# Performance work log

Hardware: AMD Instinct MI355X
Metric: run time of the kernel (lower is better)

The kernel has to match this reference:

```python
import jax, jax.numpy as jnp
import numpy as np

B, T, M, C, H = 4, 2048, 256, 512, 8
D = C // H  # head dim = 64


def _split_heads(t, n):  # [B,N,C] -> [B,H,N,D]
    b, s, c = t.shape
    return t.reshape(b, s, H, c // H).transpose(0, 2, 1, 3)


def setup_inputs() -> dict:
    key = jax.random.key(0)
    ks = jax.random.split(key, 16)
    s = 0.02
    inp = {
        "x": jax.random.normal(ks[0], (B, T, C), jnp.float32),
        "y": jax.random.normal(ks[1], (B, M, C), jnp.float32),
        "attn_x_mask": jnp.tril(jnp.ones((T, T), jnp.int32))[None, None],  # causal [1,1,T,T]
        "Wqkv_x": jax.random.normal(ks[2], (C, 3 * C), jnp.float32) * s,
        "bqkv_x": jnp.zeros((3 * C,), jnp.float32),
        "Wqkv_y": jax.random.normal(ks[3], (C, 3 * C), jnp.float32) * s,
        "bqkv_y": jnp.zeros((3 * C,), jnp.float32),
        "Wgs": jax.random.normal(ks[4], (C, C), jnp.float32) * s,
        "bgs": jnp.zeros((C,), jnp.float32),
        "Wgc": jax.random.normal(ks[5], (C, C), jnp.float32) * s,
        "bgc": jnp.zeros((C,), jnp.float32),
        "Wp": jax.random.normal(ks[6], (C, C), jnp.float32) * s,
        "bp": jnp.zeros((C,), jnp.float32),
    }
    return inp


def reference(x, y, attn_x_mask, Wqkv_x, bqkv_x, Wqkv_y, bqkv_y, Wgs, bgs, Wgc, bgc, Wp, bp):
    b, t, c = x.shape
    _, m, _ = y.shape
    scale = 1.0 / np.sqrt(D).astype(np.float32)

    qx, kx, vx = jnp.split(x @ Wqkv_x + bqkv_x, 3, axis=-1)
    qy, ky, vy = jnp.split(y @ Wqkv_y + bqkv_y, 3, axis=-1)
    qx, kx, vx = _split_heads(qx, H), _split_heads(kx, H), _split_heads(vx, H)
    qy, ky, vy = _split_heads(qy, H), _split_heads(ky, H), _split_heads(vy, H)

    # self-attn logits over x: [B,H,T,T]
    satt = jnp.einsum('bhtd,bhsd->bhts', qx, kx) * scale
    # cross scores y->x: [B,H,M,T]; bias = mean over M of softmax(dim=M)*scores -> [B,H,1,T]
    catt_y = jnp.einsum('bhmd,bhtd->bhmt', qy, kx) * scale
    bias = jnp.mean(jax.nn.softmax(catt_y, axis=-2) * catt_y, axis=-2, keepdims=True)
    satt = satt + bias  # broadcast over query rows
    satt = jnp.where(attn_x_mask == 0, -jnp.inf, satt)
    satt = jax.nn.softmax(satt, axis=-1)

    # cross-attn x->y: [B,H,T,M]
    catt = jax.nn.softmax(jnp.einsum('bhtd,bhmd->bhtm', qx, ky) * scale, axis=-1)

    sval = jnp.einsum('bhts,bhsd->bhtd', satt, vx).transpose(0, 2, 1, 3).reshape(b, t, c)
    cval = jnp.einsum('bhtm,bhmd->bhtd', catt, vy).transpose(0, 2, 1, 3).reshape(b, t, c)

    sgate = jax.nn.sigmoid(sval @ Wgs + bgs)
    cgate = jax.nn.sigmoid(cval @ Wgc + bgc)
    out = (sgate * cval + cgate * sval) @ Wp + bp
    return out
```

## Files before the change

### kernel.cpp

```cpp
#include <hip/hip_runtime.h>
#include <hip/hip_bf16.h>
#include <math.h>

#define B_ 4
#define T_ 2048
#define M_ 256
#define C_ 512
#define H_ 8
#define D_ 64
#define TC3 1536
#define QSCALE 0.125f

typedef _Float16 half_t;
typedef _Float16 half8 __attribute__((ext_vector_type(8)));
typedef _Float16 half4 __attribute__((ext_vector_type(4)));
typedef float floatx4 __attribute__((ext_vector_type(4)));

__device__ __forceinline__ void gload_lds16(const half_t* g, half_t* lds) {
  __builtin_amdgcn_global_load_lds(
      (const __attribute__((address_space(1))) unsigned int*)g,
      (__attribute__((address_space(3))) unsigned int*)(unsigned)(unsigned long long)(void*)lds,
      16, 0, 0);
}

__device__ __forceinline__ floatx4 mfma16(half8 a, half8 b, floatx4 c) {
  return __builtin_amdgcn_mfma_f32_16x16x32_f16(a, b, c, 0, 0, 0);
}
__device__ __forceinline__ floatx4 mfma16k16(half4 a, half4 b, floatx4 c) {
  return __builtin_amdgcn_mfma_f32_16x16x16f16(a, b, c, 0, 0, 0);
}

__device__ __forceinline__ half8 frag64(const half_t* lds, int row, int kc, int quad) {
  int slot = ((kc << 2) + quad) ^ (row & 7);
  return *(const half8*)(lds + row * 64 + slot * 8);
}
__device__ __forceinline__ half8 frag32(const half_t* lds, int row, int quad) {
  int slot = quad ^ ((row >> 1) & 3);
  return *(const half8*)(lds + row * 32 + slot * 8);
}

__global__ __launch_bounds__(256) void conv_all(
    const float* x, half_t* xo, const float* y, half_t* yo,
    const float* w0, const float* w1, const float* w2, const float* w3, const float* w4,
    half_t* o0, half_t* o1, half_t* o2, half_t* o3, half_t* o4) {
  __shared__ float tile[32][33];
  const int tid = threadIdx.x;
  if (blockIdx.x < 2304) {
    int blk = blockIdx.x;
    const float* src; half_t* dst; int N;
    if (blk < 768)       { src = w0; dst = o0; N = 1536; }
    else if (blk < 1536) { src = w1; dst = o1; N = 1536; blk -= 768; }
    else if (blk < 1792) { src = w2; dst = o2; N = 512;  blk -= 1536; }
    else if (blk < 2048) { src = w3; dst = o3; N = 512;  blk -= 1792; }
    else                 { src = w4; dst = o4; N = 512;  blk -= 2048; }
    const int ntx = N >> 5;
    const int tk = blk / ntx, tn = blk % ntx;
    const int r = tid >> 3, c = (tid & 7) * 4;
    float4 v = *(const float4*)(src + (size_t)(tk * 32 + r) * N + tn * 32 + c);
    tile[r][c] = v.x; tile[r][c + 1] = v.y; tile[r][c + 2] = v.z; tile[r][c + 3] = v.w;
    __syncthreads();
    half4 h;
#pragma unroll
    for (int j = 0; j < 4; ++j) h[j] = (half_t)tile[c + j][r];
    *(half4*)(dst + (size_t)(tn * 32 + r) * 512 + tk * 32 + c) = h;
  } else {
    const int nx = B_ * T_ * C_, ny = B_ * M_ * C_;
    const int n4x = nx >> 2, tot = n4x + (ny >> 2);
    int i = (blockIdx.x - 2304) * 256 + tid;
    const int stride = (gridDim.x - 2304) * 256;
    for (; i < tot; i += stride) {
      const float4* s; half_t* d; int idx;
      if (i < n4x) { s = (const float4*)x; d = xo; idx = i; }
      else { s = (const float4*)y; d = yo; idx = i - n4x; }
      float4 v = s[idx];
      half4 h; h[0] = (half_t)v.x; h[1] = (half_t)v.y; h[2] = (half_t)v.z; h[3] = (half_t)v.w;
      *(half4*)(d + idx * 4) = h;
    }
  }
}

struct GemmAcc { floatx4 a[4][4]; };

__device__ __forceinline__ void gemm_core(
    const half_t* __restrict__ A, const half_t* __restrict__ Wt,
    int rowBase, int colBase, GemmAcc& g,
    half_t* As, half_t* Bs, int tid) {
  const int lane = tid & 63, wave = tid >> 6;
  const int wm = wave >> 1, wn = wave & 1;
  const int qd = lane >> 4, lr = lane & 15;
  const int sr = lane >> 2, sc = lane & 3;
#pragma unroll
  for (int mi = 0; mi < 4; ++mi)
#pragma unroll
    for (int ni = 0; ni < 4; ++ni)
#pragma unroll
      for (int r = 0; r < 4; ++r) g.a[mi][ni][r] = 0.f;
  for (int k0 = 0; k0 < 512; k0 += 32) {
    __syncthreads();
#pragma unroll
    for (int i = 0; i < 2; ++i) {
      int r = wave * 32 + i * 16 + sr;
      int cs = sc ^ ((r >> 1) & 3);
      gload_lds16(A + (size_t)(rowBase + r) * 512 + k0 + cs * 8, As + (wave * 32 + i * 16) * 32);
      gload_lds16(Wt + (size_t)(colBase + r) * 512 + k0 + cs * 8, Bs + (wave * 32 + i * 16) * 32);
    }
    __syncthreads();
    half8 af[4], bf[4];
#pragma unroll
    for (int mi = 0; mi < 4; ++mi) af[mi] = frag32(As, wm * 64 + mi * 16 + lr, qd);
#pragma unroll
    for (int ni = 0; ni < 4; ++ni) bf[ni] = frag32(Bs, wn * 64 + ni * 16 + lr, qd);
#pragma unroll
    for (int mi = 0; mi < 4; ++mi)
#pragma unroll
      for (int ni = 0; ni < 4; ++ni)
        g.a[mi][ni] = mfma16(af[mi], bf[ni], g.a[mi][ni]);
  }
}

__global__ __launch_bounds__(256) void gemm_qkvt(
    const half_t* __restrict__ x16, const half_t* __restrict__ y16,
    const half_t* __restrict__ WxT, const half_t* __restrict__ WyT,
    const float* __restrict__ bqx, const float* __restrict__ bqy,
    half_t* __restrict__ qkvx, half_t* __restrict__ qkvy,
    half_t* __restrict__ vTx, half_t* __restrict__ vTy) {
  __shared__ __align__(16) half_t As[128 * 32];
  __shared__ __align__(16) half_t Bs[128 * 32];
  const int tid = threadIdx.x, lane = tid & 63, wave = tid >> 6;
  const int wm = wave >> 1, wn = wave & 1;
  const int qd = lane >> 4, lr = lane & 15;
  const int bxi = blockIdx.x;
  const half_t* A; const half_t* Wt; const float* bias; half_t* out;
  int rowBase, colBase, N; bool vt;
  if (bxi < 576) {
    vt = false; N = 1024;
    colBase = (bxi & 7) * 128;
    int ry = bxi >> 3;
    if (ry < 64) { A = x16; Wt = WxT; bias = bqx; out = qkvx; rowBase = ry * 128; }
    else { A = y16; Wt = WyT; bias = bqy; out = qkvy; rowBase = (ry - 64) * 128; }
  } else {
    vt = true;
    int i = bxi - 576;
    int xx = i % 18; int rest = i / 18;
    int yy = rest & 3, zz = rest >> 2;
    rowBase = yy * 128;
    if (xx < 16) {
      A = WxT + (size_t)1024 * 512; Wt = x16 + (size_t)zz * T_ * C_; bias = bqx + 1024;
      out = vTx + (size_t)zz * C_ * T_; N = T_; colBase = xx * 128;
    } else {
      A = WyT + (size_t)1024 * 512; Wt = y16 + (size_t)zz * M_ * C_; bias = bqy + 1024;
      out = vTy + (size_t)zz * C_ * M_; N = M_; colBase = (xx - 16) * 128;
    }
  }
  GemmAcc g;
  gemm_core(A, Wt, rowBase, colBase, g, As, Bs, tid);
  if (!vt) {
#pragma unroll
    for (int ni = 0; ni < 4; ++ni) {
      int col = colBase + wn * 64 + ni * 16 + lr;
      float csc = (col < 512) ? QSCALE : 1.f;
      float bc = bias[col];
#pragma unroll
      for (int mi = 0; mi < 4; ++mi) {
        int row0 = rowBase + wm * 64 + mi * 16 + qd * 4;
#pragma unroll
        for (int r = 0; r < 4; ++r)
          out[(size_t)(row0 + r) * 1024 + col] = (half_t)((g.a[mi][ni][r] + bc) * csc);
      }
    }
  } else {
#pragma unroll
    for (int ni = 0; ni < 4; ++ni) {
      int col = colBase + wn * 64 + ni * 16 + lr;
#pragma unroll
      for (int mi = 0; mi < 4; ++mi) {
        int row0 = rowBase + wm * 64 + mi * 16 + qd * 4;
#pragma unroll
        for (int r = 0; r < 4; ++r)
          out[(size_t)(row0 + r) * N + col] = (half_t)(g.a[mi][ni][r] + bias[row0 + r]);
      }
    }
  }
}

template <bool USE_BIAS, bool DO_A, bool DIAG_A, bool DIAG_B>
__device__ __forceinline__ void attn_tile_dual(
    const half_t* __restrict__ Ks, const half_t* __restrict__ Vts,
    const float* __restrict__ Bsh, const half8* qfA, const half8* qfB,
    floatx4* oA, floatx4& lacA, floatx4* oB, floatx4& lacB,
    int qd, int lr, int thresh) {
  floatx4 sA[4], sB[4];
#pragma unroll
  for (int ks = 0; ks < 4; ++ks)
#pragma unroll
    for (int r = 0; r < 4; ++r) { sA[ks][r] = 0.f; sB[ks][r] = 0.f; }
#pragma unroll
  for (int kc = 0; kc < 2; ++kc) {
#pragma unroll
    for (int ks = 0; ks < 4; ++ks) {
      half8 kfr = frag64(Ks, ks * 16 + lr, kc, qd);
      if (DO_A) sA[ks] = mfma16(kfr, qfA[kc], sA[ks]);
      sB[ks] = mfma16(kfr, qfB[kc], sB[ks]);
    }
  }
  half4 pA[4], pB[4];
#pragma unroll
  for (int ks = 0; ks < 4; ++ks) {
    floatx4 bf;
    if (USE_BIAS) bf = *(const floatx4*)(Bsh + ks * 16 + qd * 4);
#pragma unroll
    for (int r = 0; r < 4; ++r) {
      int keyl = ks * 16 + qd * 4 + r;
      if (DO_A) {
        float t = USE_BIAS ? (sA[ks][r] + bf[r]) : sA[ks][r];
        float p1 = __expf(t);
        if (DIAG_A && keyl > thresh) p1 = 0.f;
        pA[ks][r] = (half_t)p1;
      }
      float t2 = USE_BIAS ? (sB[ks][r] + bf[r]) : sB[ks][r];
      float p2 = __expf(t2);
      if (DIAG_B && keyl > thresh) p2 = 0.f;
      pB[ks][r] = (half_t)p2;
    }
  }
  const half4 ones4 = {(half_t)1.f, (half_t)1.f, (half_t)1.f, (half_t)1.f};
#pragma unroll
  for (int ks = 0; ks < 4; ++ks) {
    int slot = (ks * 2 + (qd >> 1)) ^ (lr & 7);
    const half_t* vbase = Vts + slot * 8 + (qd & 1) * 4;
#pragma unroll
    for (int dt = 0; dt < 4; ++dt) {
      half4 vf = *(const half4*)(vbase + (dt * 16 + lr) * 64);
      if (DO_A) oA[dt] = mfma16k16(pA[ks], vf, oA[dt]);
      oB[dt] = mfma16k16(pB[ks], vf, oB[dt]);
    }
    if (DO_A) lacA = mfma16k16(pA[ks], ones4, lacA);
    lacB = mfma16k16(pB[ks], ones4, lacB);
  }
}

__device__ __forceinline__ void attn_store2(
    half_t* __restrict__ dst, const floatx4* o, floatx4 lac,
    int b, int qbase, int h, int qd, int lr) {
  floatx4 inv;
#pragma unroll
  for (int r = 0; r < 4; ++r) inv[r] = 1.f / lac[r];
#pragma unroll
  for (int dt = 0; dt < 4; ++dt)
#pragma unroll
    for (int r = 0; r < 4; ++r)
      dst[(size_t)(b * T_ + qbase + qd * 4 + r) * C_ + h * D_ + dt * 16 + lr] =
          (half_t)(o[dt][r] * inv[r]);
}

__global__ __launch_bounds__(256) void bias_cross(
    const half_t* __restrict__ qkvx, const half_t* __restrict__ qkvy,
    const half_t* __restrict__ vTy, float* __restrict__ biasb,
    half_t* __restrict__ cval) {
  __shared__ __align__(16) half_t smem[24576];
  const int tid = threadIdx.x, lane = tid & 63, wave = tid >> 6;
  const int qd = lane >> 4, lr = lane & 15;
  const int rr = lane >> 3, cc = lane & 7;
  if (blockIdx.x < 512) {
    half_t* Qy = smem;
    half_t* Kx = smem + 16384;
    const int bh = blockIdx.x >> 4;
    const int tb = (blockIdx.x & 15) * 128;
    const int b = bh >> 3, h = bh & 7;
#pragma unroll
    for (int j = 0; j < 8; ++j) {
      int r = wave * 64 + j * 8 + rr;
      int cs = cc ^ (r & 7);
      gload_lds16(qkvy + (size_t)(b * M_ + r) * 1024 + h * D_ + cs * 8,
                  Qy + (wave * 64 + j * 8) * 64);
    }
#pragma unroll
    for (int j = 0; j < 4; ++j) {
      int r = wave * 32 + j * 8 + rr;
      int cs = cc ^ (r & 7);
      gload_lds16(qkvx + (size_t)(b * T_ + tb + r) * 1024 + C_ + h * D_ + cs * 8,
                  Kx + (wave * 32 + j * 8) * 64);
    }
    __syncthreads();
    half8 kf[2][2];
#pragma unroll
    for (int nt = 0; nt < 2; ++nt)
#pragma unroll
      for (int kc = 0; kc < 2; ++kc)
        kf[nt][kc] = frag64(Kx, wave * 32 + nt * 16 + lr, kc, qd);
    float ls[2] = {0.f, 0.f}, wsp[2] = {0.f, 0.f};
    for (int mt = 0; mt < 16; ++mt) {
      half8 af[2];
#pragma unroll
      for (int kc = 0; kc < 2; ++kc) af[kc] = frag64(Qy, mt * 16 + lr, kc, qd);
#pragma unroll
      for (int nt = 0; nt < 2; ++nt) {
        floatx4 s;
#pragma unroll
        for (int r = 0; r < 4; ++r) s[r] = 0.f;
#pragma unroll
        for (int kc = 0; kc < 2; ++kc) s = mfma16(af[kc], kf[nt][kc], s);
#pragma unroll
        for (int r = 0; r < 4; ++r) {
          float e = __expf(s[r]);
          ls[nt] += e;
          wsp[nt] += e * s[r];
        }
      }
    }
#pragma unroll
    for (int nt = 0; nt < 2; ++nt) {
      ls[nt] += __shfl_xor(ls[nt], 16, 64);
      ls[nt] += __shfl_xor(ls[nt], 32, 64);
      wsp[nt] += __shfl_xor(wsp[nt], 16, 64);
      wsp[nt] += __shfl_xor(wsp[nt], 32, 64);
    }
    if (qd == 0) {
#pragma unroll
      for (int nt = 0; nt < 2; ++nt)
        biasb[bh * T_ + tb + wave * 32 + nt * 16 + lr] = wsp[nt] / (256.f * ls[nt]);
    }
  } else {
    half_t* Qs  = smem;
    half_t* Ks  = smem + 8192;
    half_t* Vts = smem + 12288;
    const int idx = blockIdx.x - 512;
    const int bh = idx >> 4;
    const int qb = (idx & 15) * 128;
    const int b = bh >> 3, h = bh & 7;
#pragma unroll
    for (int j = 0; j < 4; ++j) {
      int row = wave * 32 + j * 8 + rr;
      int cs = cc ^ (row & 7);
      gload_lds16(qkvx + (size_t)(b * T_ + qb + row) * 1024 + h * D_ + cs * 8,
                  Qs + (wave * 32 + j * 8) * 64);
    }
    __syncthreads();
    half8 qfA[2], qfB[2];
#pragma unroll
    for (int kc = 0; kc < 2; ++kc) {
      qfA[kc] = frag64(Qs, wave * 32 + lr, kc, qd);
      qfB[kc] = frag64(Qs, wave * 32 + 16 + lr, kc, qd);
    }
    floatx4 oA[4], oB[4], lacA, lacB;
#pragma unroll
    for (int dt = 0; dt < 4; ++dt)
#pragma unroll
      for (int r = 0; r < 4; ++r) { oA[dt][r] = 0.f; oB[dt][r] = 0.f; }
#pragma unroll
    for (int r = 0; r < 4; ++r) { lacA[r] = 0.f; lacB[r] = 0.f; }
    for (int kt = 0; kt < 4; ++kt) {
      const int kb = kt * 64;
      __syncthreads();
#pragma unroll
      for (int j = 0; j < 2; ++j) {
        int row = wave * 16 + j * 8 + rr;
        int cs = cc ^ (row & 7);
        gload_lds16(qkvy + (size_t)(b * M_ + kb + row) * 1024 + C_ + h * D_ + cs * 8,
                    Ks + (wave * 16 + j * 8) * 64);
        gload_lds16(vTy + ((size_t)bh * 64 + row) * M_ + kb + cs * 8,
                    Vts + (wave * 16 + j * 8) * 64);
      }
      __syncthreads();
      attn_tile_dual<false, true, false, false>(Ks, Vts, nullptr, qfA, qfB,
                                                oA, lacA, oB, lacB, qd, lr, 0);
    }
    attn_store2(cval, oA, lacA, b, qb + wave * 32, h, qd, lr);
    attn_store2(cval, oB, lacB, b, qb + wave * 32 + 16, h, qd, lr);
  }
}

__global__ __launch_bounds__(256) void self_attn_part(
    const half_t* __restrict__ qkv, const half_t* __restrict__ vT,
    const float* __restrict__ biasb, float* __restrict__ partO,
    float* __restrict__ partL) {
  __shared__ __align__(16) half_t Qs[128 * 64];
  __shared__ __align__(16) half_t Ks[64 * 64];
  __shared__ __align__(16) half_t Vts[64 * 64];
  __shared__ __align__(16) float Bsh[64];
  const int tid = threadIdx.x, lane = tid & 63, wave = tid >> 6;
  const int half_ = blockIdx.x & 1;
  const int p = (blockIdx.x >> 1) & 15;
  const int bh = blockIdx.x >> 5;
  const int b = bh >> 3, h = bh & 7;
  const int qbL = p * 64, qbH = (31 - p) * 64;
  const int qd = lane >> 4, lr = lane & 15;
  const int rr = lane >> 3, cc = lane & 7;

#pragma unroll
  for (int j = 0; j < 4; ++j) {
    int rowIdx = wave * 32 + j * 8 + rr;
    int grow = (rowIdx < 64) ? (qbL + rowIdx) : (qbH + rowIdx - 64);
    int cs = cc ^ (rowIdx & 7);
    gload_lds16(qkv + (size_t)(b * T_ + grow) * 1024 + h * D_ + cs * 8,
                Qs + (wave * 32 + j * 8) * 64);
  }
  __syncthreads();
  half8 qfA[2], qfB[2];
#pragma unroll
  for (int kc = 0; kc < 2; ++kc) {
    qfA[kc] = frag64(Qs, wave * 16 + lr, kc, qd);
    qfB[kc] = frag64(Qs, 64 + wave * 16 + lr, kc, qd);
  }

  floatx4 oA[4], oB[4], lacA, lacB;
#pragma unroll
  for (int dt = 0; dt < 4; ++dt)
#pragma unroll
    for (int r = 0; r < 4; ++r) { oA[dt][r] = 0.f; oB[dt][r] = 0.f; }
#pragma unroll
  for (int r = 0; r < 4; ++r) { lacA[r] = 0.f; lacB[r] = 0.f; }
  const int thresh = wave * 16 + lr;
  const int ktEnd = 31 - p;

  for (int kt = half_; kt <= ktEnd; kt += 2) {
    const int kb = kt * 64;
    __syncthreads();
#pragma unroll
    for (int j = 0; j < 2; ++j) {
      int row = wave * 16 + j * 8 + rr;
      int cs = cc ^ (row & 7);
      gload_lds16(qkv + (size_t)(b * T_ + kb + row) * 1024 + C_ + h * D_ + cs * 8,
                  Ks + (wave * 16 + j * 8) * 64);
      gload_lds16(vT + ((size_t)bh * 64 + row) * T_ + kb + cs * 8,
                  Vts + (wave * 16 + j * 8) * 64);
    }
    if (tid < 64) Bsh[tid] = biasb[bh * T_ + kb + tid];
    __syncthreads();

    if (kt < p)
      attn_tile_dual<true, true, false, false>(Ks, Vts, Bsh, qfA, qfB, oA, lacA, oB, lacB, qd, lr, thresh);
    else if (kt == p)
      attn_tile_dual<true, true, true, false>(Ks, Vts, Bsh, qfA, qfB, oA, lacA, oB, lacB, qd, lr, thresh);
    else if (kt < ktEnd)
      attn_tile_dual<true, false, false, false>(Ks, Vts, Bsh, qfA, qfB, oA, lacA, oB, lacB, qd, lr, thresh);
    else
      attn_tile_dual<true, false, false, true>(Ks, Vts, Bsh, qfA, qfB, oA, lacA, oB, lacB, qd, lr, thresh);
  }

  const long rbase = ((long)(half_ * 32 + bh) * 16 + p) * 128;
#pragma unroll
  for (int g = 0; g < 2; ++g) {
    const floatx4* o = g ? oB : oA;
    floatx4 lac = g ? lacB : lacA;
    long rowb = rbase + g * 64 + wave * 16;
#pragma unroll
    for (int dt = 0; dt < 4; ++dt)
#pragma unroll
      for (int r = 0; r < 4; ++r)
        partO[(rowb + qd * 4 + r) * 64 + dt * 16 + lr] = o[dt][r];
    if (lr == 0) {
#pragma unroll
      for (int r = 0; r < 4; ++r) partL[rowb + qd * 4 + r] = lac[r];
    }
  }
}

__global__ __launch_bounds__(256) void self_reduce(
    const float* __restrict__ partO, const float* __restrict__ partL,
    half_t* __restrict__ sval) {
  const int bh = blockIdx.x >> 4;
  const int p = blockIdx.x & 15;
  const int b = bh >> 3, h = bh & 7;
  const int tid = threadIdx.x;
  const int c4 = tid & 15;
  const long hstrO = 32L * 16 * 128 * 64;
  const long hstrL = 32L * 16 * 128;
  const float* base0 = partO + ((long)bh * 16 + p) * 128 * 64;
  const float* base1 = base0 + hstrO;
  const float* l0 = partL + ((long)bh * 16 + p) * 128;
  const float* l1 = l0 + hstrL;
#pragma unroll
  for (int pass = 0; pass < 8; ++pass) {
    int qrow = pass * 16 + (tid >> 4);
    float4 v0 = *(const float4*)(base0 + (long)qrow * 64 + c4 * 4);
    float4 v1 = *(const float4*)(base1 + (long)qrow * 64 + c4 * 4);
    float inv = 1.f / (l0[qrow] + l1[qrow]);
    int t = (qrow < 64) ? (p * 64 + qrow) : ((31 - p) * 64 + (qrow - 64));
    half4 o;
    o[0] = (half_t)((v0.x + v1.x) * inv);
    o[1] = (half_t)((v0.y + v1.y) * inv);
    o[2] = (half_t)((v0.z + v1.z) * inv);
    o[3] = (half_t)((v0.w + v1.w) * inv);
    *(half4*)(sval + (size_t)(b * T_ + t) * 512 + h * 64 + c4 * 4) = o;
  }
}

__global__ __launch_bounds__(256) void gate_gemm64(
    const half_t* __restrict__ sv, const half_t* __restrict__ cv,
    const half_t* __restrict__ W1, const half_t* __restrict__ W2,
    const float* __restrict__ b1, const float* __restrict__ b2,
    half_t* __restrict__ z) {
  __shared__ __align__(16) half_t S1[64 * 32];
  __shared__ __align__(16) half_t S2[64 * 32];
  __shared__ __align__(16) half_t B1s[128 * 32];
  __shared__ __align__(16) half_t B2s[128 * 32];
  const int tid = threadIdx.x, lane = tid & 63, wave = tid >> 6;
  const int wm = wave >> 1, wn = wave & 1;
  const int rowBase = blockIdx.y * 64, colBase = blockIdx.x * 128;
  const int qd = lane >> 4, lr = lane & 15;
  const int sr = lane >> 2, sc = lane & 3;

  floatx4 a1[2][4], a2[2][4];
#pragma unroll
  for (int mi = 0; mi < 2; ++mi)
#pragma unroll
    for (int ni = 0; ni < 4; ++ni)
#pragma unroll
      for (int r = 0; r < 4; ++r) { a1[mi][ni][r] = 0.f; a2[mi][ni][r] = 0.f; }

  for (int k0 = 0; k0 < 512; k0 += 32) {
    __syncthreads();
    {
      int rA = wave * 16 + sr;
      int csA = sc ^ ((rA >> 1) & 3);
      gload_lds16(sv + (size_t)(rowBase + rA) * 512 + k0 + csA * 8, S1 + (wave * 16) * 32);
      gload_lds16(cv + (size_t)(rowBase + rA) * 512 + k0 + csA * 8, S2 + (wave * 16) * 32);
#pragma unroll
      for (int i = 0; i < 2; ++i) {
        int rB = i * 64 + wave * 16 + sr;
        int csB = sc ^ ((rB >> 1) & 3);
        gload_lds16(W1 + (size_t)(colBase + rB) * 512 + k0 + csB * 8, B1s + (i * 64 + wave * 16) * 32);
        gload_lds16(W2 + (size_t)(colBase + rB) * 512 + k0 + csB * 8, B2s + (i * 64 + wave * 16) * 32);
      }
    }
    __syncthreads();
    half8 af1[2], af2[2], bf1[4], bf2[4];
#pragma unroll
    for (int mi = 0; mi < 2; ++mi) {
      af1[mi] = frag32(S1, wm * 32 + mi * 16 + lr, qd);
      af2[mi] = frag32(S2, wm * 32 + mi * 16 + lr, qd);
    }
#pragma unroll
    for (int ni = 0; ni < 4; ++ni) {
      bf1[ni] = frag32(B1s, wn * 64 + ni * 16 + lr, qd);
      bf2[ni] = frag32(B2s, wn * 64 + ni * 16 + lr, qd);
    }
#pragma unroll
    for (int mi = 0; mi < 2; ++mi)
#pragma unroll
      for (int ni = 0; ni < 4; ++ni) {
        a1[mi][ni] = mfma16(af1[mi], bf1[ni], a1[mi][ni]);
        a2[mi][ni] = mfma16(af2[mi], bf2[ni], a2[mi][ni]);
      }
  }

#pragma unroll
  for (int ni = 0; ni < 4; ++ni) {
    int col = colBase + wn * 64 + ni * 16 + lr;
    float g1b = b1[col], g2b = b2[col];
#pragma unroll
    for (int mi = 0; mi < 2; ++mi) {
      int row0 = rowBase + wm * 32 + mi * 16 + qd * 4;
#pragma unroll
      for (int r = 0; r < 4; ++r) {
        size_t idx = (size_t)(row0 + r) * 512 + col;
        float sg1 = 1.f / (1.f + __expf(-(a1[mi][ni][r] + g1b)));
        float sg2 = 1.f / (1.f + __expf(-(a2[mi][ni][r] + g2b)));
        z[idx] = (half_t)(sg1 * (float)cv[idx] + sg2 * (float)sv[idx]);
      }
    }
  }
}

__global__ __launch_bounds__(256) void gemm_final64(
    const half_t* __restrict__ A, const half_t* __restrict__ Wt,
    const float* __restrict__ bias, float* __restrict__ Cout) {
  __shared__ __align__(16) half_t As[64 * 32];
  __shared__ __align__(16) half_t Bs[128 * 32];
  const int tid = threadIdx.x, lane = tid & 63, wave = tid >> 6;
  const int wm = wave >> 1, wn = wave & 1;
  const int rowBase = blockIdx.y * 64, colBase = blockIdx.x * 128;
  const int qd = lane >> 4, lr = lane & 15;
  const int sr = lane >> 2, sc = lane & 3;

  floatx4 acc[2][4];
#pragma unroll
  for (int mi = 0; mi < 2; ++mi)
#pragma unroll
    for (int ni = 0; ni < 4; ++ni)
#pragma unroll
      for (int r = 0; r < 4; ++r) acc[mi][ni][r] = 0.f;

  for (int k0 = 0; k0 < 512; k0 += 32) {
    __syncthreads();
    {
      int rA = wave * 16 + sr;
      int csA = sc ^ ((rA >> 1) & 3);
      gload_lds16(A + (size_t)(rowBase + rA) * 512 + k0 + csA * 8, As + (wave * 16) * 32);
#pragma unroll
      for (int i = 0; i < 2; ++i) {
        int rB = i * 64 + wave * 16 + sr;
        int csB = sc ^ ((rB >> 1) & 3);
        gload_lds16(Wt + (size_t)(colBase + rB) * 512 + k0 + csB * 8, Bs + (i * 64 + wave * 16) * 32);
      }
    }
    __syncthreads();
    half8 af[2], bf[4];
#pragma unroll
    for (int mi = 0; mi < 2; ++mi) af[mi] = frag32(As, wm * 32 + mi * 16 + lr, qd);
#pragma unroll
    for (int ni = 0; ni < 4; ++ni) bf[ni] = frag32(Bs, wn * 64 + ni * 16 + lr, qd);
#pragma unroll
    for (int mi = 0; mi < 2; ++mi)
#pragma unroll
      for (int ni = 0; ni < 4; ++ni)
        acc[mi][ni] = mfma16(af[mi], bf[ni], acc[mi][ni]);
  }

#pragma unroll
  for (int ni = 0; ni < 4; ++ni) {
    int col = colBase + wn * 64 + ni * 16 + lr;
    float bc = bias[col];
#pragma unroll
    for (int mi = 0; mi < 2; ++mi) {
      int row0 = rowBase + wm * 32 + mi * 16 + qd * 4;
#pragma unroll
      for (int r = 0; r < 4; ++r)
        Cout[(size_t)(row0 + r) * 512 + col] = acc[mi][ni][r] + bc;
    }
  }
}

extern "C" void kernel_launch(void* const* d_in, const int* in_sizes, int n_in,
                              void* d_out, int out_size, void* d_ws, size_t ws_size,
                              hipStream_t stream) {
  (void)in_sizes; (void)n_in; (void)out_size; (void)ws_size;
  const float* x      = (const float*)d_in[0];
  const float* y      = (const float*)d_in[1];
  const float* Wqkv_x = (const float*)d_in[3];
  const float* bqkv_x = (const float*)d_in[4];
  const float* Wqkv_y = (const float*)d_in[5];
  const float* bqkv_y = (const float*)d_in[6];
  const float* Wgs    = (const float*)d_in[7];
  const float* bgs    = (const float*)d_in[8];
  const float* Wgc    = (const float*)d_in[9];
  const float* bgc    = (const float*)d_in[10];
  const float* Wp     = (const float*)d_in[11];
  const float* bp     = (const float*)d_in[12];
  float* out = (float*)d_out;

  half_t* h = (half_t*)d_ws;
  half_t* x16    = h;  h += (size_t)B_ * T_ * C_;
  half_t* y16    = h;  h += (size_t)B_ * M_ * C_;
  half_t* WqkvxT = h;  h += (size_t)TC3 * C_;
  half_t* WqkvyT = h;  h += (size_t)TC3 * C_;
  half_t* WgsT   = h;  h += (size_t)C_ * C_;
  half_t* WgcT   = h;  h += (size_t)C_ * C_;
  half_t* WpT    = h;  h += (size_t)C_ * C_;
  half_t* qkvx   = h;  h += (size_t)B_ * T_ * 1024;
  half_t* qkvy   = h;  h += (size_t)B_ * M_ * 1024;
  half_t* vTx    = h;  h += (size_t)B_ * C_ * T_;
  half_t* vTy    = h;  h += (size_t)B_ * C_ * M_;
  half_t* sval   = h;  h += (size_t)B_ * T_ * C_;
  half_t* cval   = h;  h += (size_t)B_ * T_ * C_;
  half_t* z      = h;  h += (size_t)B_ * T_ * C_;
  float* biasb   = (float*)h;
  float* partO   = biasb + (size_t)B_ * H_ * T_;
  float* partL   = partO + 2L * 32 * 16 * 128 * 64;

  conv_all<<<3456, 256, 0, stream>>>(x, x16, y, y16,
                                     Wqkv_x, Wqkv_y, Wgs, Wgc, Wp,
                                     WqkvxT, WqkvyT, WgsT, WgcT, WpT);

  gemm_qkvt<<<864, 256, 0, stream>>>(x16, y16, WqkvxT, WqkvyT,
                                     bqkv_x, bqkv_y, qkvx, qkvy, vTx, vTy);

  bias_cross<<<1024, 256, 0, stream>>>(qkvx, qkvy, vTy, biasb, cval);

  self_attn_part<<<1024, 256, 0, stream>>>(qkvx, vTx, biasb, partO, partL);
  self_reduce<<<512, 256, 0, stream>>>(partO, partL, sval);

  gate_gemm64<<<dim3(4, 128), 256, 0, stream>>>(sval, cval, WgsT, WgcT, bgs, bgc, z);

  gemm_final64<<<dim3(4, 128), 256, 0, stream>>>(z, WpT, bp, out);
}
```

Before: 241.1 us.

## Widen GEMM K-tiles to 64 and merge split-K self-attention into one kernel

All GEMM kernels now stage 64-wide K slices into LDS with the 8-way XOR swizzle, which halves the number of barrier-separated iterations. The self-attention partial kernel and its reduction pass are replaced by a single kernel that processes two key tiles per barrier and writes normalized output directly. This removes the fp32 partial buffers and one launch, but halves the self-attention grid to 512 blocks and raises LDS use per block. The cross-attention branch also loads two K/V tiles per synchronization.

```diff
diff --git a/kernel.cpp b/kernel.cpp
--- a/kernel.cpp
+++ b/kernel.cpp
@@ -33,10 +33,6 @@
 __device__ __forceinline__ half8 frag64(const half_t* lds, int row, int kc, int quad) {
   int slot = ((kc << 2) + quad) ^ (row & 7);
   return *(const half8*)(lds + row * 64 + slot * 8);
-}
-__device__ __forceinline__ half8 frag32(const half_t* lds, int row, int quad) {
-  int slot = quad ^ ((row >> 1) & 3);
-  return *(const half8*)(lds + row * 32 + slot * 8);
 }
 
 __global__ __launch_bounds__(256) void conv_all(
@@ -81,40 +77,43 @@
 
 struct GemmAcc { floatx4 a[4][4]; };
 
-__device__ __forceinline__ void gemm_core(
+__device__ __forceinline__ void gemm_core64(
     const half_t* __restrict__ A, const half_t* __restrict__ Wt,
     int rowBase, int colBase, GemmAcc& g,
     half_t* As, half_t* Bs, int tid) {
   const int lane = tid & 63, wave = tid >> 6;
   const int wm = wave >> 1, wn = wave & 1;
   const int qd = lane >> 4, lr = lane & 15;
-  const int sr = lane >> 2, sc = lane & 3;
+  const int rr = lane >> 3, cc = lane & 7;
+  const int cs = cc ^ rr;
 #pragma unroll
   for (int mi = 0; mi < 4; ++mi)
 #pragma unroll
     for (int ni = 0; ni < 4; ++ni)
 #pragma unroll
       for (int r = 0; r < 4; ++r) g.a[mi][ni][r] = 0.f;
-  for (int k0 = 0; k0 < 512; k0 += 32) {
-    __syncthreads();
-#pragma unroll
-    for (int i = 0; i < 2; ++i) {
-      int r = wave * 32 + i * 16 + sr;
-      int cs = sc ^ ((r >> 1) & 3);
-      gload_lds16(A + (size_t)(rowBase + r) * 512 + k0 + cs * 8, As + (wave * 32 + i * 16) * 32);
-      gload_lds16(Wt + (size_t)(colBase + r) * 512 + k0 + cs * 8, Bs + (wave * 32 + i * 16) * 32);
-    }
-    __syncthreads();
-    half8 af[4], bf[4];
-#pragma unroll
-    for (int mi = 0; mi < 4; ++mi) af[mi] = frag32(As, wm * 64 + mi * 16 + lr, qd);
-#pragma unroll
-    for (int ni = 0; ni < 4; ++ni) bf[ni] = frag32(Bs, wn * 64 + ni * 16 + lr, qd);
-#pragma unroll
-    for (int mi = 0; mi < 4; ++mi)
-#pragma unroll
-      for (int ni = 0; ni < 4; ++ni)
-        g.a[mi][ni] = mfma16(af[mi], bf[ni], g.a[mi][ni]);
+  for (int k0 = 0; k0 < 512; k0 += 64) {
+    __syncthreads();
+#pragma unroll
+    for (int j = 0; j < 4; ++j) {
+      int row = wave * 32 + j * 8 + rr;
+      gload_lds16(A + (size_t)(rowBase + row) * 512 + k0 + cs * 8, As + (wave * 32 + j * 8) * 64);
+      gload_lds16(Wt + (size_t)(colBase + row) * 512 + k0 + cs * 8, Bs + (wave * 32 + j * 8) * 64);
+    }
+    __syncthreads();
+#pragma unroll
+    for (int kc = 0; kc < 2; ++kc) {
+      half8 af[4], bf[4];
+#pragma unroll
+      for (int mi = 0; mi < 4; ++mi) af[mi] = frag64(As, wm * 64 + mi * 16 + lr, kc, qd);
+#pragma unroll
+      for (int ni = 0; ni < 4; ++ni) bf[ni] = frag64(Bs, wn * 64 + ni * 16 + lr, kc, qd);
+#pragma unroll
+      for (int mi = 0; mi < 4; ++mi)
+#pragma unroll
+        for (int ni = 0; ni < 4; ++ni)
+          g.a[mi][ni] = mfma16(af[mi], bf[ni], g.a[mi][ni]);
+    }
   }
 }
 
@@ -124,8 +123,8 @@
     const float* __restrict__ bqx, const float* __restrict__ bqy,
     half_t* __restrict__ qkvx, half_t* __restrict__ qkvy,
     half_t* __restrict__ vTx, half_t* __restrict__ vTy) {
-  __shared__ __align__(16) half_t As[128 * 32];
-  __shared__ __align__(16) half_t Bs[128 * 32];
+  __shared__ __align__(16) half_t As[128 * 64];
+  __shared__ __align__(16) half_t Bs[128 * 64];
   const int tid = threadIdx.x, lane = tid & 63, wave = tid >> 6;
   const int wm = wave >> 1, wn = wave & 1;
   const int qd = lane >> 4, lr = lane & 15;
@@ -153,7 +152,7 @@
     }
   }
   GemmAcc g;
-  gemm_core(A, Wt, rowBase, colBase, g, As, Bs, tid);
+  gemm_core64(A, Wt, rowBase, colBase, g, As, Bs, tid);
   if (!vt) {
 #pragma unroll
     for (int ni = 0; ni < 4; ++ni) {
@@ -239,6 +238,22 @@
   }
 }
 
+__device__ __forceinline__ void attn_step(
+    int kt, int p, int ktEnd,
+    const half_t* Ks, const half_t* Vts, const float* Bsh,
+    const half8* qfA, const half8* qfB,
+    floatx4* oA, floatx4& lacA, floatx4* oB, floatx4& lacB,
+    int qd, int lr, int thresh) {
+  if (kt < p)
+    attn_tile_dual<true, true, false, false>(Ks, Vts, Bsh, qfA, qfB, oA, lacA, oB, lacB, qd, lr, thresh);
+  else if (kt == p)
+    attn_tile_dual<true, true, true, false>(Ks, Vts, Bsh, qfA, qfB, oA, lacA, oB, lacB, qd, lr, thresh);
+  else if (kt < ktEnd)
+    attn_tile_dual<true, false, false, false>(Ks, Vts, Bsh, qfA, qfB, oA, lacA, oB, lacB, qd, lr, thresh);
+  else
+    attn_tile_dual<true, false, false, true>(Ks, Vts, Bsh, qfA, qfB, oA, lacA, oB, lacB, qd, lr, thresh);
+}
+
 __device__ __forceinline__ void attn_store2(
     half_t* __restrict__ dst, const floatx4* o, floatx4 lac,
     int b, int qbase, int h, int qd, int lr) {
@@ -251,6 +266,80 @@
     for (int r = 0; r < 4; ++r)
       dst[(size_t)(b * T_ + qbase + qd * 4 + r) * C_ + h * D_ + dt * 16 + lr] =
           (half_t)(o[dt][r] * inv[r]);
+}
+
+__global__ __launch_bounds__(256) void self_attn_reg(
+    const half_t* __restrict__ qkv, const half_t* __restrict__ vT,
+    const float* __restrict__ biasb, half_t* __restrict__ sval) {
+  __shared__ __align__(16) half_t Qs[128 * 64];
+  __shared__ __align__(16) half_t Ks[2][64 * 64];
+  __shared__ __align__(16) half_t Vts[2][64 * 64];
+  __shared__ __align__(16) float Bsh[128];
+  const int tid = threadIdx.x, lane = tid & 63, wave = tid >> 6;
+  const int p = blockIdx.x & 15;
+  const int bh = blockIdx.x >> 4;
+  const int b = bh >> 3, h = bh & 7;
+  const int qbL = p * 64, qbH = (31 - p) * 64;
+  const int qd = lane >> 4, lr = lane & 15;
+  const int rr = lane >> 3, cc = lane & 7;
+  const int cs = cc ^ rr;
+
+#pragma unroll
+  for (int j = 0; j < 4; ++j) {
+    int rowIdx = wave * 32 + j * 8 + rr;
+    int grow = (rowIdx < 64) ? (qbL + rowIdx) : (qbH + rowIdx - 64);
+    gload_lds16(qkv + (size_t)(b * T_ + grow) * 1024 + h * D_ + cs * 8,
+                Qs + (wave * 32 + j * 8) * 64);
+  }
+  __syncthreads();
+  half8 qfA[2], qfB[2];
+#pragma unroll
+  for (int kc = 0; kc < 2; ++kc) {
+    qfA[kc] = frag64(Qs, wave * 16 + lr, kc, qd);
+    qfB[kc] = frag64(Qs, 64 + wave * 16 + lr, kc, qd);
+  }
+
+  floatx4 oA[4], oB[4], lacA, lacB;
+#pragma unroll
+  for (int dt = 0; dt < 4; ++dt)
+#pragma unroll
+    for (int r = 0; r < 4; ++r) { oA[dt][r] = 0.f; oB[dt][r] = 0.f; }
+#pragma unroll
+  for (int r = 0; r < 4; ++r) { lacA[r] = 0.f; lacB[r] = 0.f; }
+  const int thresh = wave * 16 + lr;
+  const int ktEnd = 31 - p;
+
+  for (int kt2 = 0; kt2 <= ktEnd; kt2 += 2) {
+    const bool two = (kt2 + 1 <= ktEnd);
+    __syncthreads();
+#pragma unroll
+    for (int j = 0; j < 2; ++j) {
+      int row = wave * 16 + j * 8 + rr;
+      gload_lds16(qkv + (size_t)(b * T_ + kt2 * 64 + row) * 1024 + C_ + h * D_ + cs * 8,
+                  Ks[0] + (wave * 16 + j * 8) * 64);
+      gload_lds16(vT + ((size_t)bh * 64 + row) * T_ + kt2 * 64 + cs * 8,
+                  Vts[0] + (wave * 16 + j * 8) * 64);
+    }
+    if (two) {
+#pragma unroll
+      for (int j = 0; j < 2; ++j) {
+        int row = wave * 16 + j * 8 + rr;
+        gload_lds16(qkv + (size_t)(b * T_ + kt2 * 64 + 64 + row) * 1024 + C_ + h * D_ + cs * 8,
+                    Ks[1] + (wave * 16 + j * 8) * 64);
+        gload_lds16(vT + ((size_t)bh * 64 + row) * T_ + kt2 * 64 + 64 + cs * 8,
+                    Vts[1] + (wave * 16 + j * 8) * 64);
+      }
+    }
+    if (tid < 128) Bsh[tid] = biasb[bh * T_ + kt2 * 64 + tid];
+    __syncthreads();
+
+    attn_step(kt2, p, ktEnd, Ks[0], Vts[0], Bsh, qfA, qfB, oA, lacA, oB, lacB, qd, lr, thresh);
+    if (two)
+      attn_step(kt2 + 1, p, ktEnd, Ks[1], Vts[1], Bsh + 64, qfA, qfB, oA, lacA, oB, lacB, qd, lr, thresh);
+  }
+
+  attn_store2(sval, oA, lacA, b, qbL + wave * 16, h, qd, lr);
+  attn_store2(sval, oB, lacB, b, qbH + wave * 16, h, qd, lr);
 }
 
 __global__ __launch_bounds__(256) void bias_cross(
@@ -261,6 +350,7 @@
   const int tid = threadIdx.x, lane = tid & 63, wave = tid >> 6;
   const int qd = lane >> 4, lr = lane & 15;
   const int rr = lane >> 3, cc = lane & 7;
+  const int cs = cc ^ rr;
   if (blockIdx.x < 512) {
     half_t* Qy = smem;
     half_t* Kx = smem + 16384;
@@ -270,14 +360,12 @@
 #pragma unroll
     for (int j = 0; j < 8; ++j) {
       int r = wave * 64 + j * 8 + rr;
-      int cs = cc ^ (r & 7);
       gload_lds16(qkvy + (size_t)(b * M_ + r) * 1024 + h * D_ + cs * 8,
                   Qy + (wave * 64 + j * 8) * 64);
     }
 #pragma unroll
     for (int j = 0; j < 4; ++j) {
       int r = wave * 32 + j * 8 + rr;
-      int cs = cc ^ (r & 7);
       gload_lds16(qkvx + (size_t)(b * T_ + tb + r) * 1024 + C_ + h * D_ + cs * 8,
                   Kx + (wave * 32 + j * 8) * 64);
     }
@@ -322,8 +410,10 @@
     }
   } else {
     half_t* Qs  = smem;
-    half_t* Ks  = smem + 8192;
-    half_t* Vts = smem + 12288;
+    half_t* Ks0 = smem + 8192;
+    half_t* Ks1 = smem + 12288;
+    half_t* Vt0 = smem + 16384;
+    half_t* Vt1 = smem + 20480;
     const int idx = blockIdx.x - 512;
     const int bh = idx >> 4;
     const int qb = (idx & 15) * 128;
@@ -331,7 +421,6 @@
 #pragma unroll
     for (int j = 0; j < 4; ++j) {
       int row = wave * 32 + j * 8 + rr;
-      int cs = cc ^ (row & 7);
       gload_lds16(qkvx + (size_t)(b * T_ + qb + row) * 1024 + h * D_ + cs * 8,
                   Qs + (wave * 32 + j * 8) * 64);
     }
@@ -349,140 +438,28 @@
       for (int r = 0; r < 4; ++r) { oA[dt][r] = 0.f; oB[dt][r] = 0.f; }
 #pragma unroll
     for (int r = 0; r < 4; ++r) { lacA[r] = 0.f; lacB[r] = 0.f; }
-    for (int kt = 0; kt < 4; ++kt) {
-      const int kb = kt * 64;
+    for (int kt2 = 0; kt2 < 4; kt2 += 2) {
       __syncthreads();
 #pragma unroll
       for (int j = 0; j < 2; ++j) {
         int row = wave * 16 + j * 8 + rr;
-        int cs = cc ^ (row & 7);
-        gload_lds16(qkvy + (size_t)(b * M_ + kb + row) * 1024 + C_ + h * D_ + cs * 8,
-                    Ks + (wave * 16 + j * 8) * 64);
-        gload_lds16(vTy + ((size_t)bh * 64 + row) * M_ + kb + cs * 8,
-                    Vts + (wave * 16 + j * 8) * 64);
+        gload_lds16(qkvy + (size_t)(b * M_ + kt2 * 64 + row) * 1024 + C_ + h * D_ + cs * 8,
+                    Ks0 + (wave * 16 + j * 8) * 64);
+        gload_lds16(vTy + ((size_t)bh * 64 + row) * M_ + kt2 * 64 + cs * 8,
+                    Vt0 + (wave * 16 + j * 8) * 64);
+        gload_lds16(qkvy + (size_t)(b * M_ + kt2 * 64 + 64 + row) * 1024 + C_ + h * D_ + cs * 8,
+                    Ks1 + (wave * 16 + j * 8) * 64);
+        gload_lds16(vTy + ((size_t)bh * 64 + row) * M_ + kt2 * 64 + 64 + cs * 8,
+                    Vt1 + (wave * 16 + j * 8) * 64);
       }
       __syncthreads();
-      attn_tile_dual<false, true, false, false>(Ks, Vts, nullptr, qfA, qfB,
+      attn_tile_dual<false, true, false, false>(Ks0, Vt0, nullptr, qfA, qfB,
+                                                oA, lacA, oB, lacB, qd, lr, 0);
+      attn_tile_dual<false, true, false, false>(Ks1, Vt1, nullptr, qfA, qfB,
                                                 oA, lacA, oB, lacB, qd, lr, 0);
     }
     attn_store2(cval, oA, lacA, b, qb + wave * 32, h, qd, lr);
     attn_store2(cval, oB, lacB, b, qb + wave * 32 + 16, h, qd, lr);
-  }
-}
-
-__global__ __launch_bounds__(256) void self_attn_part(
-    const half_t* __restrict__ qkv, const half_t* __restrict__ vT,
-    const float* __restrict__ biasb, float* __restrict__ partO,
-    float* __restrict__ partL) {
-  __shared__ __align__(16) half_t Qs[128 * 64];
-  __shared__ __align__(16) half_t Ks[64 * 64];
-  __shared__ __align__(16) half_t Vts[64 * 64];
-  __shared__ __align__(16) float Bsh[64];
-  const int tid = threadIdx.x, lane = tid & 63, wave = tid >> 6;
-  const int half_ = blockIdx.x & 1;
-  const int p = (blockIdx.x >> 1) & 15;
-  const int bh = blockIdx.x >> 5;
-  const int b = bh >> 3, h = bh & 7;
-  const int qbL = p * 64, qbH = (31 - p) * 64;
-  const int qd = lane >> 4, lr = lane & 15;
-  const int rr = lane >> 3, cc = lane & 7;
-
-#pragma unroll
-  for (int j = 0; j < 4; ++j) {
-    int rowIdx = wave * 32 + j * 8 + rr;
-    int grow = (rowIdx < 64) ? (qbL + rowIdx) : (qbH + rowIdx - 64);
-    int cs = cc ^ (rowIdx & 7);
-    gload_lds16(qkv + (size_t)(b * T_ + grow) * 1024 + h * D_ + cs * 8,
-                Qs + (wave * 32 + j * 8) * 64);
-  }
-  __syncthreads();
-  half8 qfA[2], qfB[2];
-#pragma unroll
-  for (int kc = 0; kc < 2; ++kc) {
-    qfA[kc] = frag64(Qs, wave * 16 + lr, kc, qd);
-    qfB[kc] = frag64(Qs, 64 + wave * 16 + lr, kc, qd);
-  }
-
-  floatx4 oA[4], oB[4], lacA, lacB;
-#pragma unroll
-  for (int dt = 0; dt < 4; ++dt)
-#pragma unroll
-    for (int r = 0; r < 4; ++r) { oA[dt][r] = 0.f; oB[dt][r] = 0.f; }
-#pragma unroll
-  for (int r = 0; r < 4; ++r) { lacA[r] = 0.f; lacB[r] = 0.f; }
-  const int thresh = wave * 16 + lr;
-  const int ktEnd = 31 - p;
-
-  for (int kt = half_; kt <= ktEnd; kt += 2) {
-    const int kb = kt * 64;
-    __syncthreads();
-#pragma unroll
-    for (int j = 0; j < 2; ++j) {
-      int row = wave * 16 + j * 8 + rr;
-      int cs = cc ^ (row & 7);
-      gload_lds16(qkv + (size_t)(b * T_ + kb + row) * 1024 + C_ + h * D_ + cs * 8,
-                  Ks + (wave * 16 + j * 8) * 64);
-      gload_lds16(vT + ((size_t)bh * 64 + row) * T_ + kb + cs * 8,
-                  Vts + (wave * 16 + j * 8) * 64);
-    }
-    if (tid < 64) Bsh[tid] = biasb[bh * T_ + kb + tid];
-    __syncthreads();
-
-    if (kt < p)
-      attn_tile_dual<true, true, false, false>(Ks, Vts, Bsh, qfA, qfB, oA, lacA, oB, lacB, qd, lr, thresh);
-    else if (kt == p)
-      attn_tile_dual<true, true, true, false>(Ks, Vts, Bsh, qfA, qfB, oA, lacA, oB, lacB, qd, lr, thresh);
-    else if (kt < ktEnd)
-      attn_tile_dual<true, false, false, false>(Ks, Vts, Bsh, qfA, qfB, oA, lacA, oB, lacB, qd, lr, thresh);
-    else
-      attn_tile_dual<true, false, false, true>(Ks, Vts, Bsh, qfA, qfB, oA, lacA, oB, lacB, qd, lr, thresh);
-  }
-
-  const long rbase = ((long)(half_ * 32 + bh) * 16 + p) * 128;
-#pragma unroll
-  for (int g = 0; g < 2; ++g) {
-    const floatx4* o = g ? oB : oA;
-    floatx4 lac = g ? lacB : lacA;
-    long rowb = rbase + g * 64 + wave * 16;
-#pragma unroll
-    for (int dt = 0; dt < 4; ++dt)
-#pragma unroll
-      for (int r = 0; r < 4; ++r)
-        partO[(rowb + qd * 4 + r) * 64 + dt * 16 + lr] = o[dt][r];
-    if (lr == 0) {
-#pragma unroll
-      for (int r = 0; r < 4; ++r) partL[rowb + qd * 4 + r] = lac[r];
-    }
-  }
-}
-
-__global__ __launch_bounds__(256) void self_reduce(
-    const float* __restrict__ partO, const float* __restrict__ partL,
-    half_t* __restrict__ sval) {
-  const int bh = blockIdx.x >> 4;
-  const int p = blockIdx.x & 15;
-  const int b = bh >> 3, h = bh & 7;
-  const int tid = threadIdx.x;
-  const int c4 = tid & 15;
-  const long hstrO = 32L * 16 * 128 * 64;
-  const long hstrL = 32L * 16 * 128;
-  const float* base0 = partO + ((long)bh * 16 + p) * 128 * 64;
-  const float* base1 = base0 + hstrO;
-  const float* l0 = partL + ((long)bh * 16 + p) * 128;
-  const float* l1 = l0 + hstrL;
-#pragma unroll
-  for (int pass = 0; pass < 8; ++pass) {
-    int qrow = pass * 16 + (tid >> 4);
-    float4 v0 = *(const float4*)(base0 + (long)qrow * 64 + c4 * 4);
-    float4 v1 = *(const float4*)(base1 + (long)qrow * 64 + c4 * 4);
-    float inv = 1.f / (l0[qrow] + l1[qrow]);
-    int t = (qrow < 64) ? (p * 64 + qrow) : ((31 - p) * 64 + (qrow - 64));
-    half4 o;
-    o[0] = (half_t)((v0.x + v1.x) * inv);
-    o[1] = (half_t)((v0.y + v1.y) * inv);
-    o[2] = (half_t)((v0.z + v1.z) * inv);
-    o[3] = (half_t)((v0.w + v1.w) * inv);
-    *(half4*)(sval + (size_t)(b * T_ + t) * 512 + h * 64 + c4 * 4) = o;
   }
 }
 
@@ -491,15 +468,16 @@
     const half_t* __restrict__ W1, const half_t* __restrict__ W2,
     const float* __restrict__ b1, const float* __restrict__ b2,
     half_t* __restrict__ z) {
-  __shared__ __align__(16) half_t S1[64 * 32];
-  __shared__ __align__(16) half_t S2[64 * 32];
-  __shared__ __align__(16) half_t B1s[128 * 32];
-  __shared__ __align__(16) half_t B2s[128 * 32];
+  __shared__ __align__(16) half_t S1[64 * 64];
+  __shared__ __align__(16) half_t S2[64 * 64];
+  __shared__ __align__(16) half_t B1s[128 * 64];
+  __shared__ __align__(16) half_t B2s[128 * 64];
   const int tid = threadIdx.x, lane = tid & 63, wave = tid >> 6;
   const int wm = wave >> 1, wn = wave & 1;
   const int rowBase = blockIdx.y * 64, colBase = blockIdx.x * 128;
   const int qd = lane >> 4, lr = lane & 15;
-  const int sr = lane >> 2, sc = lane & 3;
+  const int rr = lane >> 3, cc = lane & 7;
+  const int cs = cc ^ rr;
 
   floatx4 a1[2][4], a2[2][4];
 #pragma unroll
@@ -509,40 +487,40 @@
 #pragma unroll
       for (int r = 0; r < 4; ++r) { a1[mi][ni][r] = 0.f; a2[mi][ni][r] = 0.f; }
 
-  for (int k0 = 0; k0 < 512; k0 += 32) {
-    __syncthreads();
-    {
-      int rA = wave * 16 + sr;
-      int csA = sc ^ ((rA >> 1) & 3);
-      gload_lds16(sv + (size_t)(rowBase + rA) * 512 + k0 + csA * 8, S1 + (wave * 16) * 32);
-      gload_lds16(cv + (size_t)(rowBase + rA) * 512 + k0 + csA * 8, S2 + (wave * 16) * 32);
-#pragma unroll
-      for (int i = 0; i < 2; ++i) {
-        int rB = i * 64 + wave * 16 + sr;
-        int csB = sc ^ ((rB >> 1) & 3);
-        gload_lds16(W1 + (size_t)(colBase + rB) * 512 + k0 + csB * 8, B1s + (i * 64 + wave * 16) * 32);
-        gload_lds16(W2 + (size_t)(colBase + rB) * 512 + k0 + csB * 8, B2s + (i * 64 + wave * 16) * 32);
-      }
-    }
-    __syncthreads();
-    half8 af1[2], af2[2], bf1[4], bf2[4];
-#pragma unroll
-    for (int mi = 0; mi < 2; ++mi) {
-      af1[mi] = frag32(S1, wm * 32 + mi * 16 + lr, qd);
-      af2[mi] = frag32(S2, wm * 32 + mi * 16 + lr, qd);
-    }
-#pragma unroll
-    for (int ni = 0; ni < 4; ++ni) {
-      bf1[ni] = frag32(B1s, wn * 64 + ni * 16 + lr, qd);
-      bf2[ni] = frag32(B2s, wn * 64 + ni * 16 + lr, qd);
-    }
-#pragma unroll
-    for (int mi = 0; mi < 2; ++mi)
+  for (int k0 = 0; k0 < 512; k0 += 64) {
+    __syncthreads();
+#pragma unroll
+    for (int j = 0; j < 2; ++j) {
+      int rA = wave * 16 + j * 8 + rr;
+      gload_lds16(sv + (size_t)(rowBase + rA) * 512 + k0 + cs * 8, S1 + (wave * 16 + j * 8) * 64);
+      gload_lds16(cv + (size_t)(rowBase + rA) * 512 + k0 + cs * 8, S2 + (wave * 16 + j * 8) * 64);
+      gload_lds16(W1 + (size_t)(colBase + rA) * 512 + k0 + cs * 8, B1s + (wave * 16 + j * 8) * 64);
+      gload_lds16(W1 + (size_t)(colBase + 64 + rA) * 512 + k0 + cs * 8, B1s + (64 + wave * 16 + j * 8) * 64);
+      gload_lds16(W2 + (size_t)(colBase + rA) * 512 + k0 + cs * 8, B2s + (wave * 16 + j * 8) * 64);
+      gload_lds16(W2 + (size_t)(colBase + 64 + rA) * 512 + k0 + cs * 8, B2s + (64 + wave * 16 + j * 8) * 64);
+    }
+    __syncthreads();
+#pragma unroll
+    for (int kc = 0; kc < 2; ++kc) {
+      half8 af1[2], af2[2], bf1[4], bf2[4];
+#pragma unroll
+      for (int mi = 0; mi < 2; ++mi) {
+        af1[mi] = frag64(S1, wm * 32 + mi * 16 + lr, kc, qd);
+        af2[mi] = frag64(S2, wm * 32 + mi * 16 + lr, kc, qd);
+      }
 #pragma unroll
       for (int ni = 0; ni < 4; ++ni) {
-        a1[mi][ni] = mfma16(af1[mi], bf1[ni], a1[mi][ni]);
-        a2[mi][ni] = mfma16(af2[mi], bf2[ni], a2[mi][ni]);
-      }
+        bf1[ni] = frag64(B1s, wn * 64 + ni * 16 + lr, kc, qd);
+        bf2[ni] = frag64(B2s, wn * 64 + ni * 16 + lr, kc, qd);
+      }
+#pragma unroll
+      for (int mi = 0; mi < 2; ++mi)
+#pragma unroll
+        for (int ni = 0; ni < 4; ++ni) {
+          a1[mi][ni] = mfma16(af1[mi], bf1[ni], a1[mi][ni]);
+          a2[mi][ni] = mfma16(af2[mi], bf2[ni], a2[mi][ni]);
+        }
+    }
   }
 
 #pragma unroll
@@ -566,13 +544,14 @@
 __global__ __launch_bounds__(256) void gemm_final64(
     const half_t* __restrict__ A, const half_t* __restrict__ Wt,
     const float* __restrict__ bias, float* __restrict__ Cout) {
-  __shared__ __align__(16) half_t As[64 * 32];
-  __shared__ __align__(16) half_t Bs[128 * 32];
+  __shared__ __align__(16) half_t As[64 * 64];
+  __shared__ __align__(16) half_t Bs[128 * 64];
   const int tid = threadIdx.x, lane = tid & 63, wave = tid >> 6;
   const int wm = wave >> 1, wn = wave & 1;
   const int rowBase = blockIdx.y * 64, colBase = blockIdx.x * 128;
   const int qd = lane >> 4, lr = lane & 15;
-  const int sr = lane >> 2, sc = lane & 3;
+  const int rr = lane >> 3, cc = lane & 7;
+  const int cs = cc ^ rr;
 
   floatx4 acc[2][4];
 #pragma unroll
@@ -582,30 +561,29 @@
 #pragma unroll
       for (int r = 0; r < 4; ++r) acc[mi][ni][r] = 0.f;
 
-  for (int k0 = 0; k0 < 512; k0 += 32) {
-    __syncthreads();
-    {
-      int rA = wave * 16 + sr;
-      int csA = sc ^ ((rA >> 1) & 3);
-      gload_lds16(A + (size_t)(rowBase + rA) * 512 + k0 + csA * 8, As + (wave * 16) * 32);
-#pragma unroll
-      for (int i = 0; i < 2; ++i) {
-        int rB = i * 64 + wave * 16 + sr;
-        int csB = sc ^ ((rB >> 1) & 3);
-        gload_lds16(Wt + (size_t)(colBase + rB) * 512 + k0 + csB * 8, Bs + (i * 64 + wave * 16) * 32);
-      }
-    }
-    __syncthreads();
-    half8 af[2], bf[4];
-#pragma unroll
-    for (int mi = 0; mi < 2; ++mi) af[mi] = frag32(As, wm * 32 + mi * 16 + lr, qd);
-#pragma unroll
-    for (int ni = 0; ni < 4; ++ni) bf[ni] = frag32(Bs, wn * 64 + ni * 16 + lr, qd);
-#pragma unroll
-    for (int mi = 0; mi < 2; ++mi)
-#pragma unroll
-      for (int ni = 0; ni < 4; ++ni)
-        acc[mi][ni] = mfma16(af[mi], bf[ni], acc[mi][ni]);
+  for (int k0 = 0; k0 < 512; k0 += 64) {
+    __syncthreads();
+#pragma unroll
+    for (int j = 0; j < 2; ++j) {
+      int rA = wave * 16 + j * 8 + rr;
+      gload_lds16(A + (size_t)(rowBase + rA) * 512 + k0 + cs * 8, As + (wave * 16 + j * 8) * 64);
+      gload_lds16(Wt + (size_t)(colBase + rA) * 512 + k0 + cs * 8, Bs + (wave * 16 + j * 8) * 64);
+      gload_lds16(Wt + (size_t)(colBase + 64 + rA) * 512 + k0 + cs * 8, Bs + (64 + wave * 16 + j * 8) * 64);
+    }
+    __syncthreads();
+#pragma unroll
+    for (int kc = 0; kc < 2; ++kc) {
+      half8 af[2], bf[4];
+#pragma unroll
+      for (int mi = 0; mi < 2; ++mi) af[mi] = frag64(As, wm * 32 + mi * 16 + lr, kc, qd);
+#pragma unroll
+      for (int ni = 0; ni < 4; ++ni) bf[ni] = frag64(Bs, wn * 64 + ni * 16 + lr, kc, qd);
+#pragma unroll
+      for (int mi = 0; mi < 2; ++mi)
+#pragma unroll
+        for (int ni = 0; ni < 4; ++ni)
+          acc[mi][ni] = mfma16(af[mi], bf[ni], acc[mi][ni]);
+    }
   }
 
 #pragma unroll
@@ -656,8 +634,6 @@
   half_t* cval   = h;  h += (size_t)B_ * T_ * C_;
   half_t* z      = h;  h += (size_t)B_ * T_ * C_;
   float* biasb   = (float*)h;
-  float* partO   = biasb + (size_t)B_ * H_ * T_;
-  float* partL   = partO + 2L * 32 * 16 * 128 * 64;
 
   conv_all<<<3456, 256, 0, stream>>>(x, x16, y, y16,
                                      Wqkv_x, Wqkv_y, Wgs, Wgc, Wp,
@@ -668,8 +644,7 @@
 
   bias_cross<<<1024, 256, 0, stream>>>(qkvx, qkvy, vTy, biasb, cval);
 
-  self_attn_part<<<1024, 256, 0, stream>>>(qkvx, vTx, biasb, partO, partL);
-  self_reduce<<<512, 256, 0, stream>>>(partO, partL, sval);
+  self_attn_reg<<<512, 256, 0, stream>>>(qkvx, vTx, biasb, sval);
 
   gate_gemm64<<<dim3(4, 128), 256, 0, stream>>>(sval, cval, WgsT, WgcT, bgs, bgc, z);
 
```

Result: faster. 221.0 us (-8.4%).
